# Optimization experiments

Hardware: AMD Instinct MI355X
Metric: run time of the kernel (lower is better)

The kernel has to match this reference:

```python
import jax, jax.numpy as jnp
import numpy as np

COMMITMENT_COST = 0.25


def setup_inputs() -> dict:
    key = jax.random.key(0)
    kx, kc = jax.random.split(key)
    x = jax.random.normal(kx, (8, 32768, 8), dtype=jnp.float32)
    codebooks = jax.random.normal(kc, (8, 1024, 8), dtype=jnp.float32)  # [Q, K, D]
    return {"x": x, "codebooks": codebooks}


def reference(x, codebooks):
    # x: [B, T, D]; codebooks: [Q, K, D]
    residual = x
    quantized = jnp.zeros_like(x)
    loss = jnp.float32(0.0)
    codes = []
    num_q = codebooks.shape[0]
    for q in range(num_q):
        cb = codebooks[q]  # [K, D]
        # squared L2 distances: ||r||^2 + ||c||^2 - 2 r.c  -> [B, T, K]
        dist = (
            jnp.sum(residual * residual, axis=-1, keepdims=True)
            + jnp.sum(cb * cb, axis=-1)
            - 2.0 * jnp.einsum("btd,kd->btk", residual, cb)
        )
        idx = jnp.argmin(dist, axis=-1)  # [B, T]
        codes.append(idx)
        emb = cb[idx]  # [B, T, D] gather
        quantized = quantized + emb
        residual = residual - emb
        loss = loss + jnp.mean((jax.lax.stop_gradient(residual) - emb) ** 2)
    # straight-through estimator
    quantized = x + jax.lax.stop_gradient(quantized - x)
    return quantized, loss * COMMITMENT_COST, jnp.stack(codes)  # codes: [Q, B, T]
```

## Files before the change

kernel.cpp:

```cpp
#include <hip/hip_runtime.h>


#define TOKENS   262144
#define D        8
#define K        1024
#define Q        8
#define LOSS_OFF 2097152
#define CODES_OFF 2097153

#define BLK      256
#define GRID     (TOKENS / BLK)

typedef float v2f __attribute__((ext_vector_type(2)));

__device__ __forceinline__ float np_sum8_pureseq(const float* __restrict__ p) {
#pragma clang fp contract(off)
  float s = p[0];
  s = s + p[1]; s = s + p[2]; s = s + p[3]; s = s + p[4];
  s = s + p[5]; s = s + p[6]; s = s + p[7];
  return s;
}

__global__ __launch_bounds__(BLK) void rvq_prep(const float* __restrict__ cb,
                                                float* __restrict__ cc) {
#pragma clang fp contract(off)
  int i = blockIdx.x * BLK + threadIdx.x;
  const float* c = cb + i * D;
  float p[D];
#pragma unroll
  for (int d = 0; d < D; ++d) p[d] = c[d] * c[d];
  cc[i] = np_sum8_pureseq(p);
}

__global__ __launch_bounds__(BLK) void rvq_main(const float* __restrict__ x,
                                                const float* __restrict__ cb,
                                                const float* __restrict__ cct,
                                                float* __restrict__ out,
                                                double* __restrict__ partials) {
#pragma clang fp contract(off)
  __shared__ float sC[K][D];
  __shared__ float sCC[K];
  const int tid  = threadIdx.x;
  const int wid  = tid >> 6;
  const int lane = tid & 63;
  const int half = lane >> 5;
  const int sub  = lane & 31;
  const int t0 = blockIdx.x * 256 + wid * 64 + sub;
  const int t1 = t0 + 32;
  const int kb = half * (K / 2);

  v2f rf2[D];
  v2f qv2[D];
  {
    const float4* xa = (const float4*)(x + t0 * D);
    const float4* xb = (const float4*)(x + t1 * D);
    float4 a0 = xa[0], a1 = xa[1], b0 = xb[0], b1 = xb[1];
    rf2[0] = (v2f){a0.x, b0.x}; rf2[1] = (v2f){a0.y, b0.y};
    rf2[2] = (v2f){a0.z, b0.z}; rf2[3] = (v2f){a0.w, b0.w};
    rf2[4] = (v2f){a1.x, b1.x}; rf2[5] = (v2f){a1.y, b1.y};
    rf2[6] = (v2f){a1.z, b1.z}; rf2[7] = (v2f){a1.w, b1.w};
#pragma unroll
    for (int d = 0; d < D; ++d) qv2[d] = (v2f){0.0f, 0.0f};
  }
  double lossAcc = 0.0;

  for (int q = 0; q < Q; ++q) {
    __syncthreads();
    {
      const float4* src = (const float4*)(cb + q * (K * D));
      float4* dst = (float4*)sC;
      for (int i = tid; i < (K * D) / 4; i += BLK) dst[i] = src[i];
      const float* ccq = cct + q * K;
      for (int i = tid; i < K; i += BLK) sCC[i] = ccq[i];
    }
    __syncthreads();

    v2f rr2;
    {
      v2f p[D];
#pragma unroll
      for (int d = 0; d < D; ++d) p[d] = rf2[d] * rf2[d];
      v2f s = p[0];
      s = s + p[1]; s = s + p[2]; s = s + p[3]; s = s + p[4];
      s = s + p[5]; s = s + p[6]; s = s + p[7];
      rr2 = s;
    }

    const float* cbase = &sC[kb][0];
    const float* ccb   = &sCC[kb];
    float bestA = 3.402823466e+38f, bestB = 3.402823466e+38f;
    int ia = kb, ib = kb;
#pragma unroll 4
    for (int k = 0; k < K / 2; ++k) {
      const float4* row = (const float4*)(cbase + k * D);
      float4 ca = row[0], cb4 = row[1];
      float ccv = ccb[k];

      v2f m0 = rf2[0] * ca.x,  m1 = rf2[1] * ca.y,
          m2 = rf2[2] * ca.z,  m3 = rf2[3] * ca.w,
          m4 = rf2[4] * cb4.x, m5 = rf2[5] * cb4.y,
          m6 = rf2[6] * cb4.z, m7 = rf2[7] * cb4.w;
      v2f l0 = m0 + m4, l1 = m1 + m5, l2 = m2 + m6, l3 = m3 + m7;
      v2f dot = (l0 + l1) + (l2 + l3);
      v2f u = rr2 + ccv;
      v2f s = u - (dot + dot);
      if (s.x < bestA) { bestA = s.x; ia = kb + k; }
      if (s.y < bestB) { bestB = s.y; ib = kb + k; }
    }

    float obA = __shfl_xor(bestA, 32);
    float obB = __shfl_xor(bestB, 32);
    int   oiA = __shfl_xor(ia, 32);
    int   oiB = __shfl_xor(ib, 32);
    float loA = half ? obA : bestA,  hiA = half ? bestA : obA;
    int   liA = half ? oiA : ia,     hiiA = half ? ia : oiA;
    int idxA = (loA <= hiA) ? liA : hiiA;
    float loB = half ? obB : bestB,  hiB = half ? bestB : obB;
    int   liB = half ? oiB : ib,     hiiB = half ? ib : oiB;
    int idxB = (loB <= hiB) ? liB : hiiB;

#pragma unroll
    for (int d = 0; d < D; ++d) {
      float eA = sC[idxA][d];
      float qA = qv2[d].x + eA; qv2[d].x = qA;
      float rA = rf2[d].x - eA; rf2[d].x = rA;
      float fA = rA - eA;
      float eB = sC[idxB][d];
      float qB = qv2[d].y + eB; qv2[d].y = qB;
      float rB = rf2[d].y - eB; rf2[d].y = rB;
      float fB = rB - eB;
      if (!half) {
        lossAcc = fma((double)fA, (double)fA, lossAcc);
        lossAcc = fma((double)fB, (double)fB, lossAcc);
      }
    }
    if (!half) {
      out[CODES_OFF + q * TOKENS + t0] = (float)idxA;
      out[CODES_OFF + q * TOKENS + t1] = (float)idxB;
    }
  }

  if (!half) {
    const float4* xa = (const float4*)(x + t0 * D);
    const float4* xb = (const float4*)(x + t1 * D);
    float4 a0 = xa[0], a1 = xa[1], b0 = xb[0], b1 = xb[1];
    float xsA[D] = {a0.x, a0.y, a0.z, a0.w, a1.x, a1.y, a1.z, a1.w};
    float xsB[D] = {b0.x, b0.y, b0.z, b0.w, b1.x, b1.y, b1.z, b1.w};
    float oA[D], oB[D];
#pragma unroll
    for (int d = 0; d < D; ++d) {
      oA[d] = xsA[d] + (qv2[d].x - xsA[d]);
      oB[d] = xsB[d] + (qv2[d].y - xsB[d]);
    }
    float4 v;
    v.x = oA[0]; v.y = oA[1]; v.z = oA[2]; v.w = oA[3];
    ((float4*)(out + t0 * D))[0] = v;
    v.x = oA[4]; v.y = oA[5]; v.z = oA[6]; v.w = oA[7];
    ((float4*)(out + t0 * D))[1] = v;
    v.x = oB[0]; v.y = oB[1]; v.z = oB[2]; v.w = oB[3];
    ((float4*)(out + t1 * D))[0] = v;
    v.x = oB[4]; v.y = oB[5]; v.z = oB[6]; v.w = oB[7];
    ((float4*)(out + t1 * D))[1] = v;
  }

  for (int off = 32; off; off >>= 1) lossAcc += __shfl_down(lossAcc, off);
  __syncthreads();
  double* red = (double*)sC;
  if ((tid & 63) == 0) red[tid >> 6] = lossAcc;
  __syncthreads();
  if (tid == 0) partials[blockIdx.x] = red[0] + red[1] + red[2] + red[3];
}

__global__ __launch_bounds__(BLK) void rvq_loss(const double* __restrict__ partials,
                                                float* __restrict__ out) {
  int tid = threadIdx.x;
  double s = partials[tid] + partials[tid + BLK] +
             partials[tid + 2 * BLK] + partials[tid + 3 * BLK];
  for (int off = 32; off; off >>= 1) s += __shfl_down(s, off);
  __shared__ double red[4];
  if ((tid & 63) == 0) red[tid >> 6] = s;
  __syncthreads();
  if (tid == 0)
    out[LOSS_OFF] = (float)((red[0] + red[1] + red[2] + red[3]) *
                            (0.25 / 2097152.0));
}

extern "C" void kernel_launch(void* const* d_in, const int* in_sizes, int n_in,
                              void* d_out, int out_size, void* d_ws, size_t ws_size,
                              hipStream_t stream) {
  const float* x  = (const float*)d_in[0];
  const float* cb = (const float*)d_in[1];
  float* out = (float*)d_out;
  double* partials = (double*)d_ws;
  float* cc = (float*)(partials + GRID);

  rvq_prep<<<(Q * K) / BLK, BLK, 0, stream>>>(cb, cc);
  rvq_main<<<GRID, BLK, 0, stream>>>(x, cb, cc, out, partials);
  rvq_loss<<<1, BLK, 0, stream>>>(partials, out);
}
```

Baseline: 927.8 us.

## Transpose codebook in LDS and pack two codewords per packed-math op

Stores the per-stage codebook transposed ([D][K]) in shared memory, so each thread reads two adjacent codewords per dimension as a float2. The distance loop now packs pairs of codewords into the v2f lanes instead of pairing two tokens, and each thread processes both tokens against the same loaded codeword pair. This doubles reuse of each LDS load and uses packed FP32 math across codewords. The price is a strided, uncoalesced transposing copy from global memory each stage, and the ||r||^2 norm now uses the sequential-sum helper.

```diff
diff --git a/kernel.cpp b/kernel.cpp
--- a/kernel.cpp
+++ b/kernel.cpp
@@ -38,7 +38,7 @@
                                                 float* __restrict__ out,
                                                 double* __restrict__ partials) {
 #pragma clang fp contract(off)
-  __shared__ float sC[K][D];
+  __shared__ float sCT[D][K];
   __shared__ float sCC[K];
   const int tid  = threadIdx.x;
   const int wid  = tid >> 6;
@@ -49,63 +49,81 @@
   const int t1 = t0 + 32;
   const int kb = half * (K / 2);
 
-  v2f rf2[D];
-  v2f qv2[D];
+  float rfA[D], rfB[D], qvA[D], qvB[D];
   {
     const float4* xa = (const float4*)(x + t0 * D);
     const float4* xb = (const float4*)(x + t1 * D);
     float4 a0 = xa[0], a1 = xa[1], b0 = xb[0], b1 = xb[1];
-    rf2[0] = (v2f){a0.x, b0.x}; rf2[1] = (v2f){a0.y, b0.y};
-    rf2[2] = (v2f){a0.z, b0.z}; rf2[3] = (v2f){a0.w, b0.w};
-    rf2[4] = (v2f){a1.x, b1.x}; rf2[5] = (v2f){a1.y, b1.y};
-    rf2[6] = (v2f){a1.z, b1.z}; rf2[7] = (v2f){a1.w, b1.w};
-#pragma unroll
-    for (int d = 0; d < D; ++d) qv2[d] = (v2f){0.0f, 0.0f};
+    rfA[0] = a0.x; rfA[1] = a0.y; rfA[2] = a0.z; rfA[3] = a0.w;
+    rfA[4] = a1.x; rfA[5] = a1.y; rfA[6] = a1.z; rfA[7] = a1.w;
+    rfB[0] = b0.x; rfB[1] = b0.y; rfB[2] = b0.z; rfB[3] = b0.w;
+    rfB[4] = b1.x; rfB[5] = b1.y; rfB[6] = b1.z; rfB[7] = b1.w;
+#pragma unroll
+    for (int d = 0; d < D; ++d) { qvA[d] = 0.0f; qvB[d] = 0.0f; }
   }
   double lossAcc = 0.0;
 
   for (int q = 0; q < Q; ++q) {
     __syncthreads();
     {
-      const float4* src = (const float4*)(cb + q * (K * D));
-      float4* dst = (float4*)sC;
-      for (int i = tid; i < (K * D) / 4; i += BLK) dst[i] = src[i];
+      const float* cbq = cb + q * (K * D);
+      float* flat = (float*)sCT;
+      for (int i = tid; i < K * D; i += BLK)
+        flat[i] = cbq[(i & (K - 1)) * D + (i >> 10)];
       const float* ccq = cct + q * K;
       for (int i = tid; i < K; i += BLK) sCC[i] = ccq[i];
     }
     __syncthreads();
 
-    v2f rr2;
+    float rrA, rrB;
     {
-      v2f p[D];
-#pragma unroll
-      for (int d = 0; d < D; ++d) p[d] = rf2[d] * rf2[d];
-      v2f s = p[0];
-      s = s + p[1]; s = s + p[2]; s = s + p[3]; s = s + p[4];
-      s = s + p[5]; s = s + p[6]; s = s + p[7];
-      rr2 = s;
-    }
-
-    const float* cbase = &sC[kb][0];
-    const float* ccb   = &sCC[kb];
+      float p[D];
+#pragma unroll
+      for (int d = 0; d < D; ++d) p[d] = rfA[d] * rfA[d];
+      rrA = np_sum8_pureseq(p);
+#pragma unroll
+      for (int d = 0; d < D; ++d) p[d] = rfB[d] * rfB[d];
+      rrB = np_sum8_pureseq(p);
+    }
+    v2f rrA2 = (v2f){rrA, rrA}, rrB2 = (v2f){rrB, rrB};
+    v2f rf2A[D], rf2B[D];
+#pragma unroll
+    for (int d = 0; d < D; ++d) {
+      rf2A[d] = (v2f){rfA[d], rfA[d]};
+      rf2B[d] = (v2f){rfB[d], rfB[d]};
+    }
+
     float bestA = 3.402823466e+38f, bestB = 3.402823466e+38f;
     int ia = kb, ib = kb;
-#pragma unroll 4
-    for (int k = 0; k < K / 2; ++k) {
-      const float4* row = (const float4*)(cbase + k * D);
-      float4 ca = row[0], cb4 = row[1];
-      float ccv = ccb[k];
-
-      v2f m0 = rf2[0] * ca.x,  m1 = rf2[1] * ca.y,
-          m2 = rf2[2] * ca.z,  m3 = rf2[3] * ca.w,
-          m4 = rf2[4] * cb4.x, m5 = rf2[5] * cb4.y,
-          m6 = rf2[6] * cb4.z, m7 = rf2[7] * cb4.w;
-      v2f l0 = m0 + m4, l1 = m1 + m5, l2 = m2 + m6, l3 = m3 + m7;
-      v2f dot = (l0 + l1) + (l2 + l3);
-      v2f u = rr2 + ccv;
-      v2f s = u - (dot + dot);
-      if (s.x < bestA) { bestA = s.x; ia = kb + k; }
-      if (s.y < bestB) { bestB = s.y; ib = kb + k; }
+    const float* ccb = &sCC[kb];
+#pragma unroll 2
+    for (int kp = 0; kp < K / 4; ++kp) {
+      const int k = kb + kp * 2;
+      v2f cd[D];
+#pragma unroll
+      for (int d = 0; d < D; ++d)
+        cd[d] = *(const v2f*)&sCT[d][k];
+      v2f cc2 = *(const v2f*)&ccb[kp * 2];
+
+      v2f a0 = rf2A[0] * cd[0], a1 = rf2A[1] * cd[1],
+          a2 = rf2A[2] * cd[2], a3 = rf2A[3] * cd[3],
+          a4 = rf2A[4] * cd[4], a5 = rf2A[5] * cd[5],
+          a6 = rf2A[6] * cd[6], a7 = rf2A[7] * cd[7];
+      v2f La0 = a0 + a4, La1 = a1 + a5, La2 = a2 + a6, La3 = a3 + a7;
+      v2f dA = (La0 + La1) + (La2 + La3);
+      v2f sA = (rrA2 + cc2) - (dA + dA);
+      if (sA.x < bestA) { bestA = sA.x; ia = k; }
+      if (sA.y < bestA) { bestA = sA.y; ia = k + 1; }
+
+      v2f b0 = rf2B[0] * cd[0], b1 = rf2B[1] * cd[1],
+          b2 = rf2B[2] * cd[2], b3 = rf2B[3] * cd[3],
+          b4 = rf2B[4] * cd[4], b5 = rf2B[5] * cd[5],
+          b6 = rf2B[6] * cd[6], b7 = rf2B[7] * cd[7];
+      v2f Lb0 = b0 + b4, Lb1 = b1 + b5, Lb2 = b2 + b6, Lb3 = b3 + b7;
+      v2f dB = (Lb0 + Lb1) + (Lb2 + Lb3);
+      v2f sB = (rrB2 + cc2) - (dB + dB);
+      if (sB.x < bestB) { bestB = sB.x; ib = k; }
+      if (sB.y < bestB) { bestB = sB.y; ib = k + 1; }
     }
 
     float obA = __shfl_xor(bestA, 32);
@@ -121,14 +139,14 @@
 
 #pragma unroll
     for (int d = 0; d < D; ++d) {
-      float eA = sC[idxA][d];
-      float qA = qv2[d].x + eA; qv2[d].x = qA;
-      float rA = rf2[d].x - eA; rf2[d].x = rA;
-      float fA = rA - eA;
-      float eB = sC[idxB][d];
-      float qB = qv2[d].y + eB; qv2[d].y = qB;
-      float rB = rf2[d].y - eB; rf2[d].y = rB;
-      float fB = rB - eB;
+      float eA = sCT[d][idxA];
+      qvA[d] = qvA[d] + eA;
+      rfA[d] = rfA[d] - eA;
+      float fA = rfA[d] - eA;
+      float eB = sCT[d][idxB];
+      qvB[d] = qvB[d] + eB;
+      rfB[d] = rfB[d] - eB;
+      float fB = rfB[d] - eB;
       if (!half) {
         lossAcc = fma((double)fA, (double)fA, lossAcc);
         lossAcc = fma((double)fB, (double)fB, lossAcc);
@@ -149,8 +167,8 @@
     float oA[D], oB[D];
 #pragma unroll
     for (int d = 0; d < D; ++d) {
-      oA[d] = xsA[d] + (qv2[d].x - xsA[d]);
-      oB[d] = xsB[d] + (qv2[d].y - xsB[d]);
+      oA[d] = xsA[d] + (qvA[d] - xsA[d]);
+      oB[d] = xsB[d] + (qvB[d] - xsB[d]);
     }
     float4 v;
     v.x = oA[0]; v.y = oA[1]; v.z = oA[2]; v.w = oA[3];
@@ -165,7 +183,7 @@
 
   for (int off = 32; off; off >>= 1) lossAcc += __shfl_down(lossAcc, off);
   __syncthreads();
-  double* red = (double*)sC;
+  double* red = (double*)sCT;
   if ((tid & 63) == 0) red[tid >> 6] = lossAcc;
   __syncthreads();
   if (tid == 0) partials[blockIdx.x] = red[0] + red[1] + red[2] + red[3];
```

Result: faster. 885.0 us (median of 2 runs) (-4.6%).
